# Kernel optimization log

Measured on AMD Instinct MI355X. Metric: run time of the kernel, lower is better.

Reference implementation:

```python
import jax, jax.numpy as jnp
import numpy as np

IMG = 512
STRIDES = (8, 16, 32, 64, 128)
AREAS = np.array([(IMG // s) ** 2 for s in STRIDES])  # [4096,1024,256,64,16]
A_TOTAL = int(AREAS.sum())  # 5456
LEVELS = 5
TOP_K = 3
MAX_OBJ = 32
NUM_CLASSES = 80
BATCH = 16


def _detections():
    # [LEVELS, A_TOTAL] one-hot level membership per anchor (tf.pad of ones)
    det = np.zeros((LEVELS, A_TOTAL), np.float32)
    off = 0
    for i, a in enumerate(AREAS):
        det[i, off:off + a] = 1.0
        off += a
    return jnp.asarray(det)


def focal_loss(y_true, y_pred, alpha=0.25, gamma=2.0):
    # y_pred are sigmoid probabilities; sum over classes -> [B, A]
    p = jnp.clip(y_pred, 1e-7, 1.0 - 1e-7)
    ce = -(y_true * jnp.log(p) + (1.0 - y_true) * jnp.log(1.0 - p))
    alpha_t = y_true * alpha + (1.0 - y_true) * (1.0 - alpha)
    pt = y_true * (1.0 - p) + (1.0 - y_true) * p
    return jnp.sum(alpha_t * pt ** gamma * ce, axis=-1)


def giou_loss(y_true, y_pred):
    # ltrb distance encoding (all >= 0) -> per-anchor GIoU loss [B, A]
    tl, tt, tr, tb = (y_true[..., i] for i in range(4))
    pl, pt_, pr, pb = (y_pred[..., i] for i in range(4))
    area_t = (tl + tr) * (tt + tb)
    area_p = (pl + pr) * (pt_ + pb)
    inter = (jnp.minimum(tl, pl) + jnp.minimum(tr, pr)) * (jnp.minimum(tt, pt_) + jnp.minimum(tb, pb))
    union = area_t + area_p - inter
    iou = inter / jnp.maximum(union, 1e-7)
    enc = (jnp.maximum(tl, pl) + jnp.maximum(tr, pr)) * (jnp.maximum(tt, pt_) + jnp.maximum(tb, pb))
    giou = iou - (enc - union) / jnp.maximum(enc, 1e-7)
    return 1.0 - giou


def dwlm(total_loss, ind, bbox_cnt):
    # total_loss [B,A], ind [B,A] int, bbox_cnt [B] int
    det = _detections()                                   # [L, A]
    obj_ids = jnp.arange(MAX_OBJ)                         # [O]
    valid = obj_ids[None, :] < bbox_cnt[:, None]          # [B, O]
    obj_mask = (ind[:, None, :] == obj_ids[None, :, None]).astype(total_loss.dtype)  # [B,O,A]
    det_mask = obj_mask[:, :, None, :] * det[None, None]  # [B,O,L,A]
    obj_l_sum = jnp.einsum('ba,bola->bol', total_loss, det_mask)
    cnt = jnp.sum(det_mask, axis=-1)                      # [B,O,L]
    mean = obj_l_sum / jnp.maximum(1.0, cnt)
    lmax = jnp.max(mean, axis=-1, keepdims=True) + 1e-5
    mean = jnp.where(mean == 0.0, lmax, mean)
    lmin = jnp.min(mean, axis=-1, keepdims=True)
    target = 1.0 - (mean - lmin) / (lmax - lmin)          # [B,O,L]
    kth = jax.lax.top_k(target, TOP_K)[0][..., -1:]
    target = jnp.where(target >= kth, target, 0.0)
    target = jnp.where(valid[..., None], target, 0.0)     # drop padded objects
    return jnp.einsum('bol,bola->ba', target, det_mask)   # scatter-sum back to anchors


def setup_inputs() -> dict:
    key = jax.random.key(0)
    k = jax.random.split(key, 6)
    return {
        'cls_pred': jax.random.uniform(k[0], (BATCH, A_TOTAL, NUM_CLASSES), jnp.float32),
        'loc_pred': jax.random.uniform(k[1], (BATCH, A_TOTAL, 4), jnp.float32),
        'cls_tar': jax.random.uniform(k[2], (BATCH, A_TOTAL, NUM_CLASSES + 2), jnp.float32),
        'loc_tar': jax.random.uniform(k[3], (BATCH, A_TOTAL, 4), jnp.float32),
        'ind_tar': jax.random.randint(k[4], (BATCH, A_TOTAL, 1), 0, MAX_OBJ, jnp.int32),
        'bboxes_cnt': jax.random.randint(k[5], (BATCH, 1), 0, MAX_OBJ, jnp.int32),
    }


def reference(cls_pred, loc_pred, cls_tar, loc_tar, ind_tar, bboxes_cnt):
    cls_loss = focal_loss(cls_tar[..., :-2], cls_pred)
    loc_loss = giou_loss(loc_tar, loc_pred)
    dwlm_out = dwlm(cls_loss + loc_loss, ind_tar[..., 0], bboxes_cnt[..., 0])
    pos_mask = cls_tar[..., -1]
    dwlm_out_masked = jnp.where(pos_mask > 0.0, dwlm_out, 1.0)
    return dwlm_out_masked[..., None], pos_mask
```

## Files before the change

kernel.cpp:

```cpp
#include <hip/hip_runtime.h>

constexpr int A_TOTAL = 5456;
constexpr int BATCH = 16;
constexpr int NUM_CLASSES = 80;
constexpr int NUM_CH = NUM_CLASSES + 2;
constexpr int MAX_OBJ = 32;
constexpr int LEVELS = 5;
constexpr int BINS = MAX_OBJ * LEVELS;
constexpr int BLK_L = 1024;
constexpr int NSLOT = 16;
constexpr int APB = A_TOTAL / NSLOT;
constexpr int PASS = BLK_L / 4;
constexpr int BLK_G = 256;
constexpr int NBLK_G = (A_TOTAL + BLK_G - 1) / BLK_G;
constexpr float LN2 = 0.69314718056f;

__device__ __forceinline__ int lev_of(int a) {
    return (a < 4096) ? 0 : (a < 5120) ? 1 : (a < 5376) ? 2 : (a < 5440) ? 3 : 4;
}

__device__ __forceinline__ float focal20(const float4* p4, const float4* t4) {
    float fl = 0.f;
    #pragma unroll
    for (int jj = 0; jj < 5; ++jj) {
        float ps[4] = {p4[jj].x, p4[jj].y, p4[jj].z, p4[jj].w};
        float ts[4] = {t4[jj].x, t4[jj].y, t4[jj].z, t4[jj].w};
        #pragma unroll
        for (int k = 0; k < 4; ++k) {
            float p  = fminf(fmaxf(ps[k], 1e-7f), 1.0f - 1e-7f);
            float tt = ts[k];
            float lp = __log2f(p);
            float lq = __log2f(1.0f - p);
            float ce2 = tt * (lp - lq) + lq;
            float alpha_t = 0.75f - 0.5f * tt;
            float pt = tt * (1.0f - 2.0f * p) + p;
            fl += alpha_t * pt * pt * ce2;
        }
    }
    return fl;
}

__global__ void __launch_bounds__(BLK_L)
loss_accum_kernel(const float* __restrict__ cls_pred,
                  const float* __restrict__ loc_pred,
                  const float* __restrict__ cls_tar,
                  const float* __restrict__ loc_tar,
                  const int*   __restrict__ ind_tar,
                  float* __restrict__ p_sum,
                  float* __restrict__ p_cnt,
                  float* __restrict__ out) {
    __shared__ float s_sum[BINS];
    __shared__ float s_cnt[BINS];
    const int t = threadIdx.x;
    if (t < BINS) { s_sum[t] = 0.f; s_cnt[t] = 0.f; }
    __syncthreads();

    const int b = blockIdx.y;
    const int j = blockIdx.x;
    const int q = t & 3;
    const int r = t >> 2;

    const int a1 = j * APB + r;
    const int a2 = a1 + PASS;
    const bool v2 = (r + PASS) < APB;
    const size_t row1 = (size_t)b * A_TOTAL + a1;
    const size_t row2 = row1 + PASS;

    const char* predb = (const char*)cls_pred;
    const char* tarb  = (const char*)cls_tar;
    float4 p4a[5], t4a[5], p4b[5], t4b[5];
    {
        const float4* pp1 = (const float4*)(predb + row1 * 320 + q * 16);
        const float4* tt1 = (const float4*)(tarb  + row1 * 328 + q * 16);
        #pragma unroll
        for (int jj = 0; jj < 5; ++jj) { p4a[jj] = pp1[jj * 4]; t4a[jj] = tt1[jj * 4]; }
    }
    float4 T1, P1, T2, P2;
    float pos1 = 0.f, pos2 = 0.f;
    T1 = ((const float4*)(loc_tar  + row1 * 4))[0];
    P1 = ((const float4*)(loc_pred + row1 * 4))[0];
    pos1 = cls_tar[row1 * NUM_CH + (NUM_CH - 1)];
    if (v2) {
        const float4* pp2 = (const float4*)(predb + row2 * 320 + q * 16);
        const float4* tt2 = (const float4*)(tarb  + row2 * 328 + q * 16);
        #pragma unroll
        for (int jj = 0; jj < 5; ++jj) { p4b[jj] = pp2[jj * 4]; t4b[jj] = tt2[jj * 4]; }
        T2 = ((const float4*)(loc_tar  + row2 * 4))[0];
        P2 = ((const float4*)(loc_pred + row2 * 4))[0];
        pos2 = cls_tar[row2 * NUM_CH + (NUM_CH - 1)];
    }

    float fl = focal20(p4a, t4a);
    fl += __shfl_xor(fl, 1);
    fl += __shfl_xor(fl, 2);
    if (q == 0) {
        out[(size_t)BATCH * A_TOTAL + row1] = pos1;
        float area_t = (T1.x + T1.z) * (T1.y + T1.w);
        float area_p = (P1.x + P1.z) * (P1.y + P1.w);
        float inter  = (fminf(T1.x, P1.x) + fminf(T1.z, P1.z)) * (fminf(T1.y, P1.y) + fminf(T1.w, P1.w));
        float uni    = area_t + area_p - inter;
        float iou    = inter / fmaxf(uni, 1e-7f);
        float enc    = (fmaxf(T1.x, P1.x) + fmaxf(T1.z, P1.z)) * (fmaxf(T1.y, P1.y) + fmaxf(T1.w, P1.w));
        float giou   = iou - (enc - uni) / fmaxf(enc, 1e-7f);
        float loss   = (1.f - giou) - LN2 * fl;
        int bin = ind_tar[row1] * LEVELS + lev_of(a1);
        atomicAdd(&s_sum[bin], loss);
        atomicAdd(&s_cnt[bin], 1.0f);
    }

    if (v2) {
        float fl2 = focal20(p4b, t4b);
        fl2 += __shfl_xor(fl2, 1);
        fl2 += __shfl_xor(fl2, 2);
        if (q == 0) {
            out[(size_t)BATCH * A_TOTAL + row2] = pos2;
            float area_t = (T2.x + T2.z) * (T2.y + T2.w);
            float area_p = (P2.x + P2.z) * (P2.y + P2.w);
            float inter  = (fminf(T2.x, P2.x) + fminf(T2.z, P2.z)) * (fminf(T2.y, P2.y) + fminf(T2.w, P2.w));
            float uni    = area_t + area_p - inter;
            float iou    = inter / fmaxf(uni, 1e-7f);
            float enc    = (fmaxf(T2.x, P2.x) + fmaxf(T2.z, P2.z)) * (fmaxf(T2.y, P2.y) + fmaxf(T2.w, P2.w));
            float giou   = iou - (enc - uni) / fmaxf(enc, 1e-7f);
            float loss   = (1.f - giou) - LN2 * fl2;
            int bin = ind_tar[row2] * LEVELS + lev_of(a2);
            atomicAdd(&s_sum[bin], loss);
            atomicAdd(&s_cnt[bin], 1.0f);
        }
    }

    __syncthreads();
    if (t < BINS) {
        const size_t slot = ((size_t)b * NSLOT + j) * BINS + t;
        p_sum[slot] = s_sum[t];
        p_cnt[slot] = s_cnt[t];
    }
}

__global__ void __launch_bounds__(BLK_G)
gather_kernel(const float* __restrict__ p_sum,
              const float* __restrict__ p_cnt,
              const int*   __restrict__ ind_tar,
              const int*   __restrict__ bbox_cnt,
              float* __restrict__ out) {
    __shared__ float s_mean[BINS];
    __shared__ float s_tgt[BINS];
    const int t = threadIdx.x;
    const int b = blockIdx.y;

    if (t < BINS) {
        float s = 0.f, c = 0.f;
        const size_t base = (size_t)b * NSLOT * BINS + t;
        #pragma unroll
        for (int k = 0; k < NSLOT; ++k) {
            s += p_sum[base + (size_t)k * BINS];
            c += p_cnt[base + (size_t)k * BINS];
        }
        s_mean[t] = s / fmaxf(1.0f, c);
    }
    __syncthreads();

    if (t < MAX_OBJ) {
        float mean[LEVELS];
        float mx = -1e30f;
        #pragma unroll
        for (int l = 0; l < LEVELS; ++l) {
            mean[l] = s_mean[t * LEVELS + l];
            mx = fmaxf(mx, mean[l]);
        }
        float lmax = mx + 1e-5f;
        float mn = 1e30f;
        #pragma unroll
        for (int l = 0; l < LEVELS; ++l) {
            if (mean[l] == 0.0f) mean[l] = lmax;
            mn = fminf(mn, mean[l]);
        }
        float denom = lmax - mn;
        float tgt[LEVELS];
        float m1 = -1e30f, m2 = -1e30f, m3 = -1e30f;
        #pragma unroll
        for (int l = 0; l < LEVELS; ++l) {
            float v = 1.0f - (mean[l] - mn) / denom;
            tgt[l] = v;
            if (v > m1)      { m3 = m2; m2 = m1; m1 = v; }
            else if (v > m2) { m3 = m2; m2 = v; }
            else if (v > m3) { m3 = v; }
        }
        const bool valid = t < bbox_cnt[b];
        #pragma unroll
        for (int l = 0; l < LEVELS; ++l) {
            float v = tgt[l];
            v = (v >= m3) ? v : 0.0f;
            s_tgt[t * LEVELS + l] = valid ? v : 0.0f;
        }
    }
    __syncthreads();

    const int a = blockIdx.x * BLK_G + t;
    if (a >= A_TOTAL) return;
    const size_t row = (size_t)b * A_TOTAL + a;
    float pos = out[(size_t)BATCH * A_TOTAL + row];
    int o = ind_tar[row];
    out[row] = (pos > 0.0f) ? s_tgt[o * LEVELS + lev_of(a)] : 1.0f;
}

extern "C" void kernel_launch(void* const* d_in, const int* in_sizes, int n_in,
                              void* d_out, int out_size, void* d_ws, size_t ws_size,
                              hipStream_t stream) {
    const float* cls_pred = (const float*)d_in[0];
    const float* loc_pred = (const float*)d_in[1];
    const float* cls_tar  = (const float*)d_in[2];
    const float* loc_tar  = (const float*)d_in[3];
    const int*   ind_tar  = (const int*)d_in[4];
    const int*   bbox_cnt = (const int*)d_in[5];
    float* out = (float*)d_out;

    float* p_sum = (float*)d_ws;
    float* p_cnt = p_sum + (size_t)BATCH * NSLOT * BINS;

    loss_accum_kernel<<<dim3(NSLOT, BATCH), dim3(BLK_L), 0, stream>>>(
        cls_pred, loc_pred, cls_tar, loc_tar, ind_tar, p_sum, p_cnt, out);
    gather_kernel<<<dim3(NBLK_G, BATCH), dim3(BLK_G), 0, stream>>>(
        p_sum, p_cnt, ind_tar, bbox_cnt, out);
}
```

Baseline: 20.08 us.

## Fuse loss accumulation and gather into one kernel via last-block election

Merges the two kernels into one. Each block atomically adds its per-bin partial sums into global buffers and bumps a per-batch counter. The last block of each batch then computes the level targets and writes all anchor outputs, which saves a second kernel launch and the partial-buffer reduction. In exchange it adds a memset launch, global atomics, and a serial tail where a single block per batch writes all 5456 outputs. The memory ordering relies on atomics and has no explicit fence.

```diff
diff --git a/kernel.cpp b/kernel.cpp
--- a/kernel.cpp
+++ b/kernel.cpp
@@ -11,8 +11,6 @@
 constexpr int NSLOT = 16;
 constexpr int APB = A_TOTAL / NSLOT;
 constexpr int PASS = BLK_L / 4;
-constexpr int BLK_G = 256;
-constexpr int NBLK_G = (A_TOTAL + BLK_G - 1) / BLK_G;
 constexpr float LN2 = 0.69314718056f;
 
 __device__ __forceinline__ int lev_of(int a) {
@@ -41,16 +39,20 @@
 }
 
 __global__ void __launch_bounds__(BLK_L)
-loss_accum_kernel(const float* __restrict__ cls_pred,
+fused_dwlm_kernel(const float* __restrict__ cls_pred,
                   const float* __restrict__ loc_pred,
                   const float* __restrict__ cls_tar,
                   const float* __restrict__ loc_tar,
                   const int*   __restrict__ ind_tar,
-                  float* __restrict__ p_sum,
-                  float* __restrict__ p_cnt,
+                  const int*   __restrict__ bbox_cnt,
+                  float* __restrict__ g_sum,
+                  float* __restrict__ g_cnt,
+                  unsigned int* __restrict__ counters,
                   float* __restrict__ out) {
     __shared__ float s_sum[BINS];
     __shared__ float s_cnt[BINS];
+    __shared__ float s_tgt[BINS];
+    __shared__ int   s_last;
     const int t = threadIdx.x;
     if (t < BINS) { s_sum[t] = 0.f; s_cnt[t] = 0.f; }
     __syncthreads();
@@ -127,35 +129,27 @@
             atomicAdd(&s_cnt[bin], 1.0f);
         }
     }
-
-    __syncthreads();
+    __syncthreads();
+
     if (t < BINS) {
-        const size_t slot = ((size_t)b * NSLOT + j) * BINS + t;
-        p_sum[slot] = s_sum[t];
-        p_cnt[slot] = s_cnt[t];
-    }
-}
-
-__global__ void __launch_bounds__(BLK_G)
-gather_kernel(const float* __restrict__ p_sum,
-              const float* __restrict__ p_cnt,
-              const int*   __restrict__ ind_tar,
-              const int*   __restrict__ bbox_cnt,
-              float* __restrict__ out) {
-    __shared__ float s_mean[BINS];
-    __shared__ float s_tgt[BINS];
-    const int t = threadIdx.x;
-    const int b = blockIdx.y;
+        float c = s_cnt[t];
+        if (c != 0.f) {
+            atomicAdd(&g_sum[b * BINS + t], s_sum[t]);
+            atomicAdd(&g_cnt[b * BINS + t], c);
+        }
+    }
+    __syncthreads();
+    if (t == 0) {
+        unsigned int old = atomicAdd(&counters[b], 1u);
+        s_last = (old == NSLOT - 1);
+    }
+    __syncthreads();
+    if (!s_last) return;
 
     if (t < BINS) {
-        float s = 0.f, c = 0.f;
-        const size_t base = (size_t)b * NSLOT * BINS + t;
-        #pragma unroll
-        for (int k = 0; k < NSLOT; ++k) {
-            s += p_sum[base + (size_t)k * BINS];
-            c += p_cnt[base + (size_t)k * BINS];
-        }
-        s_mean[t] = s / fmaxf(1.0f, c);
+        float s = atomicAdd(&g_sum[b * BINS + t], 0.0f);
+        float c = atomicAdd(&g_cnt[b * BINS + t], 0.0f);
+        s_sum[t] = s / fmaxf(1.0f, c);
     }
     __syncthreads();
 
@@ -164,7 +158,7 @@
         float mx = -1e30f;
         #pragma unroll
         for (int l = 0; l < LEVELS; ++l) {
-            mean[l] = s_mean[t * LEVELS + l];
+            mean[l] = s_sum[t * LEVELS + l];
             mx = fmaxf(mx, mean[l]);
         }
         float lmax = mx + 1e-5f;
@@ -185,22 +179,32 @@
             else if (v > m2) { m3 = m2; m2 = v; }
             else if (v > m3) { m3 = v; }
         }
-        const bool valid = t < bbox_cnt[b];
+        const bool vld = t < bbox_cnt[b];
         #pragma unroll
         for (int l = 0; l < LEVELS; ++l) {
             float v = tgt[l];
             v = (v >= m3) ? v : 0.0f;
-            s_tgt[t * LEVELS + l] = valid ? v : 0.0f;
-        }
-    }
-    __syncthreads();
-
-    const int a = blockIdx.x * BLK_G + t;
-    if (a >= A_TOTAL) return;
-    const size_t row = (size_t)b * A_TOTAL + a;
-    float pos = out[(size_t)BATCH * A_TOTAL + row];
-    int o = ind_tar[row];
-    out[row] = (pos > 0.0f) ? s_tgt[o * LEVELS + lev_of(a)] : 1.0f;
+            s_tgt[t * LEVELS + l] = vld ? v : 0.0f;
+        }
+    }
+    __syncthreads();
+
+    {
+        float posv[6];
+        int   ov[6], av[6];
+        int n = 0;
+        for (int a3 = t; a3 < A_TOTAL; a3 += BLK_L) {
+            const size_t r3 = (size_t)b * A_TOTAL + a3;
+            posv[n] = cls_tar[r3 * NUM_CH + (NUM_CH - 1)];
+            ov[n]   = ind_tar[r3];
+            av[n]   = a3;
+            ++n;
+        }
+        for (int i = 0; i < n; ++i) {
+            const size_t r3 = (size_t)b * A_TOTAL + av[i];
+            out[r3] = (posv[i] > 0.0f) ? s_tgt[ov[i] * LEVELS + lev_of(av[i])] : 1.0f;
+        }
+    }
 }
 
 extern "C" void kernel_launch(void* const* d_in, const int* in_sizes, int n_in,
@@ -214,11 +218,15 @@
     const int*   bbox_cnt = (const int*)d_in[5];
     float* out = (float*)d_out;
 
-    float* p_sum = (float*)d_ws;
-    float* p_cnt = p_sum + (size_t)BATCH * NSLOT * BINS;
-
-    loss_accum_kernel<<<dim3(NSLOT, BATCH), dim3(BLK_L), 0, stream>>>(
-        cls_pred, loc_pred, cls_tar, loc_tar, ind_tar, p_sum, p_cnt, out);
-    gather_kernel<<<dim3(NBLK_G, BATCH), dim3(BLK_G), 0, stream>>>(
-        p_sum, p_cnt, ind_tar, bbox_cnt, out);
-}
+    float* g_sum = (float*)d_ws;
+    float* g_cnt = g_sum + (size_t)BATCH * BINS;
+    unsigned int* counters = (unsigned int*)(g_cnt + (size_t)BATCH * BINS);
+
+    hipMemsetAsync(d_ws, 0,
+                   (2 * BATCH * BINS) * sizeof(float) + BATCH * sizeof(unsigned int),
+                   stream);
+
+    fused_dwlm_kernel<<<dim3(NSLOT, BATCH), dim3(BLK_L), 0, stream>>>(
+        cls_pred, loc_pred, cls_tar, loc_tar, ind_tar, bbox_cnt,
+        g_sum, g_cnt, counters, out);
+}
```

After: 32.21 us. 60.4% more time.
